# Optimization experiments

Hardware: AMD Instinct MI355X
Metric: run time of the kernel (lower is better)

## Reference

```python
import jax, jax.numpy as jnp
import numpy as np

N_NODES = 100000
D_IN = 64
D_OUT = 64
N_EDGES = 1250000


def setup_inputs() -> dict:
    key = jax.random.key(0)
    k_x, k_e, k_wl, k_bl, k_wr = jax.random.split(key, 5)
    x = jax.random.normal(k_x, (N_NODES, D_IN), dtype=jnp.float32)
    edge_index = jax.random.randint(k_e, (2, N_EDGES), 0, N_NODES, dtype=jnp.int64)
    # SAGEConv params: lin_l (neighbor transform, with bias), lin_r (root transform, no bias)
    s_in = 1.0 / np.sqrt(D_IN)
    W_l = jax.random.uniform(k_wl, (D_IN, D_OUT), dtype=jnp.float32, minval=-s_in, maxval=s_in)
    b_l = jax.random.uniform(k_bl, (D_OUT,), dtype=jnp.float32, minval=-s_in, maxval=s_in)
    W_r = jax.random.uniform(k_wr, (D_IN, D_OUT), dtype=jnp.float32, minval=-s_in, maxval=s_in)
    return {"x": x, "edge_index": edge_index, "W_l": W_l, "b_l": b_l, "W_r": W_r}


def reference(x, edge_index, W_l, b_l, W_r):
    # PyG SAGEConv with aggr='add':
    #   out = lin_l(sum_{j in N(i)} x_j) + lin_r(x_i), then tanh
    src = edge_index[0]  # message sources (x_j)
    dst = edge_index[1]  # message targets (i)
    msg = x[src]                                             # [E, D_IN] gather
    aggr = jax.ops.segment_sum(msg, dst, num_segments=x.shape[0])  # [N, D_IN] scatter-add
    out = aggr @ W_l + b_l + x @ W_r                         # [N, D_OUT]
    return jnp.tanh(out)
```

## Files before the change

kernel.cpp:

```cpp
#include <hip/hip_runtime.h>
#include <hip/hip_bf16.h>
#include <hip/hip_fp16.h>

#define N_NODES 100000
#define D 64
#define N_EDGES 1250000

#define RB 64
#define NB 1563
#define FCAP 1536
#define SORT_CAP 1536

#define CB_SHIFT 11
#define NCB 49
#define CCAP 28672
#define FINE_PER_COARSE 32

#define CPAD 16

#define EPB 8192
#define PARTA_BLOCKS ((N_EDGES + EPB - 1) / EPB)
#define SEGS 16
#define SEG_CAP 1792

#define TNP 256
#define PRE_BLOCKS ((N_NODES + TNP - 1) / TNP)
#define FUSED_BLOCKS (PARTA_BLOCKS + PRE_BLOCKS)

#define NWAVE 16

#define XP 72
#define SMEM_BYTES 55296

#define SG_BPB 2
#define SG_BLOCKS ((NB + SG_BPB - 1) / SG_BPB)

typedef unsigned short ushort_t;
typedef _Float16 half_t;
typedef __attribute__((ext_vector_type(8))) _Float16 half8;
typedef __attribute__((ext_vector_type(4))) float floatx4;

__global__ __launch_bounds__(1024) void pre_part_kernel(
    const float* __restrict__ x, const float* __restrict__ W_l,
    const float* __restrict__ b_l, const float* __restrict__ W_r,
    ushort_t* __restrict__ y, ushort_t* __restrict__ z,
    const int* __restrict__ src, const int* __restrict__ dst,
    int* __restrict__ ccursor, unsigned* __restrict__ coarse,
    int N, int E)
{
    extern __shared__ char smem[];
    int t = threadIdx.x;

    if (blockIdx.x < PARTA_BLOCKS) {
        int* hist16       = (int*)smem;
        int* lbase        = (int*)(smem + 3200);
        int* gbase        = (int*)(smem + 3456);
        int* lwb          = (int*)(smem + 3712);
        unsigned* sortedL = (unsigned*)(smem + 6912);
        const int w = t >> 6;

        if (t < NWAVE * NCB) hist16[t] = 0;
        __syncthreads();

        int base = blockIdx.x * EPB;
        int lim = E - base; if (lim > EPB) lim = EPB;

        for (int i = t; i < lim; i += 1024)
            atomicAdd(&hist16[w * NCB + (dst[base + i] >> CB_SHIFT)], 1);
        __syncthreads();

        if (t < 64) {
            int cw[NWAVE]; int tot = 0;
            if (t < NCB) {
#pragma unroll
                for (int k = 0; k < NWAVE; k++) { cw[k] = hist16[k * NCB + t]; tot += cw[k]; }
            }
            int inc = tot;
#pragma unroll
            for (int off = 1; off < 64; off <<= 1) {
                int n = __shfl_up(inc, off, 64);
                if (t >= off) inc += n;
            }
            int ex = inc - tot;
            if (t < NCB) {
                lbase[t] = ex;
                gbase[t] = tot ? atomicAdd(&ccursor[t * CPAD], tot) : 0;
                int run = ex;
#pragma unroll
                for (int k = 0; k < NWAVE; k++) { lwb[k * NCB + t] = run; run += cw[k]; }
            } else {
                lbase[t] = lim;
            }
        }
        __syncthreads();

        for (int i = t; i < lim; i += 1024) {
            int d = dst[base + i];
            int s = src[base + i];
            int b = d >> CB_SHIFT;
            int pos = atomicSub(&hist16[w * NCB + b], 1) - 1;
            sortedL[lwb[w * NCB + b] + pos] =
                (unsigned)s | ((unsigned)(d & ((1 << CB_SHIFT) - 1)) << 17);
        }
        __syncthreads();

        for (int i = t; i < lim; i += 1024) {
            int lo = 0;
#pragma unroll
            for (int s2 = 32; s2; s2 >>= 1) {
                int c = lo + s2;
                if (c < 64 && lbase[c] <= i) lo = c;
            }
            coarse[(size_t)lo * CCAP + gbase[lo] + (i - lbase[lo])] = sortedL[i];
        }
        return;
    }

    half_t* sWt = (half_t*)smem;
    half_t* sXh = (half_t*)(smem + 18432);

    for (int i = t; i < 64 * 64; i += 1024) {
        int k = i >> 6, c = i & 63;
        sWt[c * XP + k]        = (half_t)W_l[i];
        sWt[(64 + c) * XP + k] = (half_t)W_r[i];
    }

    long base = (long)(blockIdx.x - PARTA_BLOCKS) * TNP;
    for (int i = t; i < TNP * 16; i += 1024) {
        int n = i >> 4, q = i & 15;
        long node = base + n;
        float4 v = make_float4(0.f, 0.f, 0.f, 0.f);
        if (node < N) v = ((const float4*)(x + node * D))[q];
        half_t* p = &sXh[n * XP + q * 4];
        p[0] = (half_t)v.x; p[1] = (half_t)v.y;
        p[2] = (half_t)v.z; p[3] = (half_t)v.w;
    }
    __syncthreads();

    const int lane  = t & 63;
    const int w     = t >> 6;
    const int col16 = lane & 15;
    const int quad  = lane >> 4;

    const int nrow = w * 16 + col16;
    half8 xb0 = *(half8*)&sXh[nrow * XP + quad * 8];
    half8 xb1 = *(half8*)&sXh[nrow * XP + 32 + quad * 8];

    float4 bq[4];
#pragma unroll
    for (int j = 0; j < 4; j++) bq[j] = *(const float4*)(b_l + j * 16 + quad * 4);

#pragma unroll
    for (int ct = 0; ct < 4; ct++) {
        int c = ct * 16 + col16;
        half8 wa0 = *(half8*)&sWt[c * XP + quad * 8];
        half8 wa1 = *(half8*)&sWt[c * XP + 32 + quad * 8];
        floatx4 acc = {0.f, 0.f, 0.f, 0.f};
        acc = __builtin_amdgcn_mfma_f32_16x16x32_f16(wa0, xb0, acc, 0, 0, 0);
        acc = __builtin_amdgcn_mfma_f32_16x16x32_f16(wa1, xb1, acc, 0, 0, 0);
        union { half_t h[4]; uint2 u; } pk;
        pk.h[0] = (half_t)acc[0]; pk.h[1] = (half_t)acc[1];
        pk.h[2] = (half_t)acc[2]; pk.h[3] = (half_t)acc[3];
        *(uint2*)&sXh[nrow * XP + ct * 16 + quad * 4] = pk.u;
    }
    __syncthreads();

    for (int c2 = t; c2 < TNP * 8; c2 += 1024) {
        int row = c2 >> 3, f = c2 & 7;
        if (base + row < N)
            *(uint4*)(y + (base + row) * D + f * 8) = *(uint4*)&sXh[row * XP + f * 8];
    }
    __syncthreads();

#pragma unroll
    for (int ct = 4; ct < 8; ct++) {
        int c = ct * 16 + col16;
        half8 wa0 = *(half8*)&sWt[c * XP + quad * 8];
        half8 wa1 = *(half8*)&sWt[c * XP + 32 + quad * 8];
        floatx4 acc = {0.f, 0.f, 0.f, 0.f};
        acc = __builtin_amdgcn_mfma_f32_16x16x32_f16(wa0, xb0, acc, 0, 0, 0);
        acc = __builtin_amdgcn_mfma_f32_16x16x32_f16(wa1, xb1, acc, 0, 0, 0);
        float4 bv = bq[ct - 4];
        union { half_t h[4]; uint2 u; } pk;
        pk.h[0] = (half_t)(acc[0] + bv.x); pk.h[1] = (half_t)(acc[1] + bv.y);
        pk.h[2] = (half_t)(acc[2] + bv.z); pk.h[3] = (half_t)(acc[3] + bv.w);
        *(uint2*)&sXh[nrow * XP + (ct - 4) * 16 + quad * 4] = pk.u;
    }
    __syncthreads();

    for (int c2 = t; c2 < TNP * 8; c2 += 1024) {
        int row = c2 >> 3, f = c2 & 7;
        if (base + row < N)
            *(uint4*)(z + (base + row) * D + f * 8) = *(uint4*)&sXh[row * XP + f * 8];
    }
}

__global__ __launch_bounds__(256) void partB_kernel(
    const unsigned* __restrict__ coarse, const int* __restrict__ ccursor,
    int* __restrict__ fcursor, unsigned* __restrict__ fine)
{
    __shared__ int hist4[4 * FINE_PER_COARSE];
    __shared__ int lbase2[FINE_PER_COARSE];
    __shared__ int gbase2[FINE_PER_COARSE];
    __shared__ int lwb2[4 * FINE_PER_COARSE];
    __shared__ unsigned sortedL[SEG_CAP];

    int cb = blockIdx.x >> 4;
    int seg = blockIdx.x & 15;
    int t = threadIdx.x;
    const int w = t >> 6;

    int cnt = ccursor[cb * CPAD];
    int segLen = (cnt + SEGS - 1) / SEGS;
    int beg = seg * segLen;
    int end = beg + segLen; if (end > cnt) end = cnt;
    int lim = end - beg; if (lim < 0) lim = 0;

    if (t < 4 * FINE_PER_COARSE) hist4[t] = 0;
    __syncthreads();

    const unsigned* __restrict__ slab = coarse + (size_t)cb * CCAP + beg;

    for (int i = t; i < lim; i += 256)
        atomicAdd(&hist4[w * FINE_PER_COARSE + ((slab[i] >> 17) >> 6)], 1);
    __syncthreads();

    if (t < 64) {
        int c0 = 0, c1 = 0, c2 = 0, c3 = 0, tot = 0;
        if (t < FINE_PER_COARSE) {
            c0 = hist4[t]; c1 = hist4[FINE_PER_COARSE + t];
            c2 = hist4[2 * FINE_PER_COARSE + t]; c3 = hist4[3 * FINE_PER_COARSE + t];
            tot = c0 + c1 + c2 + c3;
        }
        int inc = tot;
#pragma unroll
        for (int off = 1; off < 32; off <<= 1) {
            int n = __shfl_up(inc, off, 64);
            if (t >= off) inc += n;
        }
        int ex = inc - tot;
        if (t < FINE_PER_COARSE) {
            lbase2[t] = ex;
            int fb = cb * FINE_PER_COARSE + t;
            gbase2[t] = tot ? atomicAdd(&fcursor[fb * CPAD], tot) : 0;
            lwb2[t]                       = ex;
            lwb2[FINE_PER_COARSE + t]     = ex + c0;
            lwb2[2 * FINE_PER_COARSE + t] = ex + c0 + c1;
            lwb2[3 * FINE_PER_COARSE + t] = ex + c0 + c1 + c2;
        }
    }
    __syncthreads();

    for (int i = t; i < lim; i += 256) {
        unsigned e = slab[i];
        unsigned cl = e >> 17;
        int loc = cl >> 6;
        int pos = atomicSub(&hist4[w * FINE_PER_COARSE + loc], 1) - 1;
        sortedL[lwb2[w * FINE_PER_COARSE + loc] + pos] =
            (e & 0x1FFFFu) | ((cl & 63u) << 17);
    }
    __syncthreads();

    for (int i = t; i < lim; i += 256) {
        int lo = 0;
#pragma unroll
        for (int s2 = 16; s2; s2 >>= 1) {
            int c = lo + s2;
            if (c < FINE_PER_COARSE && lbase2[c] <= i) lo = c;
        }
        fine[((size_t)cb * FINE_PER_COARSE + lo) * FCAP + gbase2[lo] + (i - lbase2[lo])]
            = sortedL[i];
    }
}

__global__ __launch_bounds__(512) void sortgather_kernel(
    const ushort_t* __restrict__ y, const ushort_t* __restrict__ z,
    const unsigned* __restrict__ part, const int* __restrict__ cursor,
    float* __restrict__ out, int N)
{
    __shared__ int sorted[SORT_CAP];
    __shared__ int hist[RB];
    __shared__ int cur[RB];
    __shared__ int begL[RB];

    int t = threadIdx.x;

    for (int sub = 0; sub < SG_BPB; sub++) {
        int b = blockIdx.x * SG_BPB + sub;
        if (b >= NB) break;
        __syncthreads();

        int cnt = cursor[b * CPAD];
        if (cnt > SORT_CAP) cnt = SORT_CAP;
        const unsigned* __restrict__ slab = part + (size_t)b * FCAP;

        unsigned e0 = 0, e1 = 0, e2 = 0;
        int i0 = t, i1 = t + 512, i2 = t + 1024;
        if (i0 < cnt) e0 = slab[i0];
        if (i1 < cnt) e1 = slab[i1];
        if (i2 < cnt) e2 = slab[i2];

        if (t < RB) hist[t] = 0;
        __syncthreads();

        if (i0 < cnt) atomicAdd(&hist[e0 >> 17], 1);
        if (i1 < cnt) atomicAdd(&hist[e1 >> 17], 1);
        if (i2 < cnt) atomicAdd(&hist[e2 >> 17], 1);
        __syncthreads();

        if (t < RB) {
            int v = hist[t];
            int inc = v;
#pragma unroll
            for (int off = 1; off < RB; off <<= 1) {
                int n = __shfl_up(inc, off, RB);
                if (t >= off) inc += n;
            }
            int ex = inc - v;
            cur[t] = ex;
            begL[t] = ex;
        }
        __syncthreads();

        if (i0 < cnt) { int p = atomicAdd(&cur[e0 >> 17], 1); sorted[p] = (int)(e0 & 0x1FFFF); }
        if (i1 < cnt) { int p = atomicAdd(&cur[e1 >> 17], 1); sorted[p] = (int)(e1 & 0x1FFFF); }
        if (i2 < cnt) { int p = atomicAdd(&cur[e2 >> 17], 1); sorted[p] = (int)(e2 & 0x1FFFF); }
        __syncthreads();

        const int g = t >> 3;
        const int f = t & 7;
        int myBeg = begL[g];
        int myDeg = hist[g];

        float2 acc0 = make_float2(0.f, 0.f), acc1 = acc0, acc2 = acc0, acc3 = acc0;

#define ACC(r) { \
        float2 c0 = __half22float2(*(const __half2*)&(r).x); \
        float2 c1 = __half22float2(*(const __half2*)&(r).y); \
        float2 c2 = __half22float2(*(const __half2*)&(r).z); \
        float2 c3 = __half22float2(*(const __half2*)&(r).w); \
        acc0.x += c0.x; acc0.y += c0.y; acc1.x += c1.x; acc1.y += c1.y; \
        acc2.x += c2.x; acc2.y += c2.y; acc3.x += c3.x; acc3.y += c3.y; }

        int i = 0;
        for (; i + 8 <= myDeg; i += 8) {
            int s0 = sorted[myBeg + i];
            int s1 = sorted[myBeg + i + 1];
            int s2 = sorted[myBeg + i + 2];
            int s3 = sorted[myBeg + i + 3];
            int s4 = sorted[myBeg + i + 4];
            int s5 = sorted[myBeg + i + 5];
            int s6 = sorted[myBeg + i + 6];
            int s7 = sorted[myBeg + i + 7];
            uint4 r0 = ((const uint4*)(y + (size_t)s0 * D))[f];
            uint4 r1 = ((const uint4*)(y + (size_t)s1 * D))[f];
            uint4 r2 = ((const uint4*)(y + (size_t)s2 * D))[f];
            uint4 r3 = ((const uint4*)(y + (size_t)s3 * D))[f];
            uint4 r4 = ((const uint4*)(y + (size_t)s4 * D))[f];
            uint4 r5 = ((const uint4*)(y + (size_t)s5 * D))[f];
            uint4 r6 = ((const uint4*)(y + (size_t)s6 * D))[f];
            uint4 r7 = ((const uint4*)(y + (size_t)s7 * D))[f];
            ACC(r0) ACC(r1) ACC(r2) ACC(r3) ACC(r4) ACC(r5) ACC(r6) ACC(r7)
        }
        for (; i + 4 <= myDeg; i += 4) {
            int s0 = sorted[myBeg + i];
            int s1 = sorted[myBeg + i + 1];
            int s2 = sorted[myBeg + i + 2];
            int s3 = sorted[myBeg + i + 3];
            uint4 r0 = ((const uint4*)(y + (size_t)s0 * D))[f];
            uint4 r1 = ((const uint4*)(y + (size_t)s1 * D))[f];
            uint4 r2 = ((const uint4*)(y + (size_t)s2 * D))[f];
            uint4 r3 = ((const uint4*)(y + (size_t)s3 * D))[f];
            ACC(r0) ACC(r1) ACC(r2) ACC(r3)
        }
        for (; i < myDeg; i++) {
            int s = sorted[myBeg + i];
            uint4 r = ((const uint4*)(y + (size_t)s * D))[f];
            ACC(r)
        }
#undef ACC

        long gn = (long)b * RB + g;
        if (gn < N) {
            uint4 zr = ((const uint4*)(z + (size_t)gn * D))[f];
            float2 z0 = __half22float2(*(const __half2*)&zr.x);
            float2 z1 = __half22float2(*(const __half2*)&zr.y);
            float2 z2 = __half22float2(*(const __half2*)&zr.z);
            float2 z3 = __half22float2(*(const __half2*)&zr.w);
            float4 o0, o1;
            o0.x = tanhf(acc0.x + z0.x); o0.y = tanhf(acc0.y + z0.y);
            o0.z = tanhf(acc1.x + z1.x); o0.w = tanhf(acc1.y + z1.y);
            o1.x = tanhf(acc2.x + z2.x); o1.y = tanhf(acc2.y + z2.y);
            o1.z = tanhf(acc3.x + z3.x); o1.w = tanhf(acc3.y + z3.y);
            float4* op = (float4*)(out + gn * D);
            op[2 * f] = o0;
            op[2 * f + 1] = o1;
        }
    }
}

extern "C" void kernel_launch(void* const* d_in, const int* in_sizes, int n_in,
                              void* d_out, int out_size, void* d_ws, size_t ws_size,
                              hipStream_t stream) {
    const float* x   = (const float*)d_in[0];
    const int* ei    = (const int*)d_in[1];
    const float* W_l = (const float*)d_in[2];
    const float* b_l = (const float*)d_in[3];
    const float* W_r = (const float*)d_in[4];
    float* out = (float*)d_out;

    const int N = N_NODES;
    const int E = N_EDGES;
    const int* src = ei;
    const int* dst = ei + E;

    char* ws = (char*)d_ws;
    ushort_t* y      = (ushort_t*)(ws);
    ushort_t* z      = (ushort_t*)(ws + 12800000);
    unsigned* coarse = (unsigned*)(ws + 25600000);
    unsigned* fine   = (unsigned*)(ws + 31219712);
    int* ccursor     = (int*)(ws + 40822784);
    int* fcursor     = (int*)(ws + 40825920);

    hipMemsetAsync(ccursor, 0, 103168, stream);

    pre_part_kernel<<<FUSED_BLOCKS, 1024, SMEM_BYTES, stream>>>(
        x, W_l, b_l, W_r, y, z, src, dst, ccursor, coarse, N, E);
    partB_kernel<<<NCB * SEGS, 256, 0, stream>>>(coarse, ccursor, fcursor, fine);
    sortgather_kernel<<<SG_BLOCKS, 512, 0, stream>>>(y, z, fine, fcursor, out, N);
}
```

Before: 138.7 us.

## Scatter coarse partition directly to global and make pre-GEMM wave-local

```diff
diff --git a/kernel.cpp b/kernel.cpp
--- a/kernel.cpp
+++ b/kernel.cpp
@@ -26,7 +26,6 @@
 #define TNP 256
 #define PRE_BLOCKS ((N_NODES + TNP - 1) / TNP)
 #define FUSED_BLOCKS (PARTA_BLOCKS + PRE_BLOCKS)
-
 #define NWAVE 16
 
 #define XP 72
@@ -52,11 +51,8 @@
     int t = threadIdx.x;
 
     if (blockIdx.x < PARTA_BLOCKS) {
-        int* hist16       = (int*)smem;
-        int* lbase        = (int*)(smem + 3200);
-        int* gbase        = (int*)(smem + 3456);
-        int* lwb          = (int*)(smem + 3712);
-        unsigned* sortedL = (unsigned*)(smem + 6912);
+        int* hist16 = (int*)smem;
+        int* lwb16  = (int*)(smem + 3200);
         const int w = t >> 6;
 
         if (t < NWAVE * NCB) hist16[t] = 0;
@@ -69,28 +65,13 @@
             atomicAdd(&hist16[w * NCB + (dst[base + i] >> CB_SHIFT)], 1);
         __syncthreads();
 
-        if (t < 64) {
+        if (t < NCB) {
             int cw[NWAVE]; int tot = 0;
-            if (t < NCB) {
-#pragma unroll
-                for (int k = 0; k < NWAVE; k++) { cw[k] = hist16[k * NCB + t]; tot += cw[k]; }
-            }
-            int inc = tot;
-#pragma unroll
-            for (int off = 1; off < 64; off <<= 1) {
-                int n = __shfl_up(inc, off, 64);
-                if (t >= off) inc += n;
-            }
-            int ex = inc - tot;
-            if (t < NCB) {
-                lbase[t] = ex;
-                gbase[t] = tot ? atomicAdd(&ccursor[t * CPAD], tot) : 0;
-                int run = ex;
-#pragma unroll
-                for (int k = 0; k < NWAVE; k++) { lwb[k * NCB + t] = run; run += cw[k]; }
-            } else {
-                lbase[t] = lim;
-            }
+#pragma unroll
+            for (int k = 0; k < NWAVE; k++) { cw[k] = hist16[k * NCB + t]; tot += cw[k]; }
+            int g = tot ? atomicAdd(&ccursor[t * CPAD], tot) : 0;
+#pragma unroll
+            for (int k = 0; k < NWAVE; k++) { lwb16[k * NCB + t] = g; g += cw[k]; }
         }
         __syncthreads();
 
@@ -99,19 +80,8 @@
             int s = src[base + i];
             int b = d >> CB_SHIFT;
             int pos = atomicSub(&hist16[w * NCB + b], 1) - 1;
-            sortedL[lwb[w * NCB + b] + pos] =
+            coarse[(size_t)b * CCAP + lwb16[w * NCB + b] + pos] =
                 (unsigned)s | ((unsigned)(d & ((1 << CB_SHIFT) - 1)) << 17);
-        }
-        __syncthreads();
-
-        for (int i = t; i < lim; i += 1024) {
-            int lo = 0;
-#pragma unroll
-            for (int s2 = 32; s2; s2 >>= 1) {
-                int c = lo + s2;
-                if (c < 64 && lbase[c] <= i) lo = c;
-            }
-            coarse[(size_t)lo * CCAP + gbase[lo] + (i - lbase[lo])] = sortedL[i];
         }
         return;
     }
@@ -125,30 +95,38 @@
         sWt[(64 + c) * XP + k] = (half_t)W_r[i];
     }
 
-    long base = (long)(blockIdx.x - PARTA_BLOCKS) * TNP;
-    for (int i = t; i < TNP * 16; i += 1024) {
-        int n = i >> 4, q = i & 15;
-        long node = base + n;
-        float4 v = make_float4(0.f, 0.f, 0.f, 0.f);
-        if (node < N) v = ((const float4*)(x + node * D))[q];
-        half_t* p = &sXh[n * XP + q * 4];
-        p[0] = (half_t)v.x; p[1] = (half_t)v.y;
-        p[2] = (half_t)v.z; p[3] = (half_t)v.w;
-    }
-    __syncthreads();
-
     const int lane  = t & 63;
     const int w     = t >> 6;
     const int col16 = lane & 15;
     const int quad  = lane >> 4;
 
+    float4 bq[4];
+#pragma unroll
+    for (int j = 0; j < 4; j++) bq[j] = *(const float4*)(b_l + j * 16 + quad * 4);
+
+    __syncthreads();
+
+    long base = (long)(blockIdx.x - PARTA_BLOCKS) * TNP;
+
+    {
+        int rl = w * 16 + (lane >> 2);
+        long node = base + rl;
+        bool ok = node < N;
+        int qb = lane & 3;
+#pragma unroll
+        for (int k = 0; k < 4; k++) {
+            int q = qb + k * 4;
+            float4 v = make_float4(0.f, 0.f, 0.f, 0.f);
+            if (ok) v = ((const float4*)(x + node * D))[q];
+            half_t* p = &sXh[rl * XP + q * 4];
+            p[0] = (half_t)v.x; p[1] = (half_t)v.y;
+            p[2] = (half_t)v.z; p[3] = (half_t)v.w;
+        }
+    }
+
     const int nrow = w * 16 + col16;
     half8 xb0 = *(half8*)&sXh[nrow * XP + quad * 8];
     half8 xb1 = *(half8*)&sXh[nrow * XP + 32 + quad * 8];
-
-    float4 bq[4];
-#pragma unroll
-    for (int j = 0; j < 4; j++) bq[j] = *(const float4*)(b_l + j * 16 + quad * 4);
 
 #pragma unroll
     for (int ct = 0; ct < 4; ct++) {
@@ -163,14 +141,17 @@
         pk.h[2] = (half_t)acc[2]; pk.h[3] = (half_t)acc[3];
         *(uint2*)&sXh[nrow * XP + ct * 16 + quad * 4] = pk.u;
     }
-    __syncthreads();
-
-    for (int c2 = t; c2 < TNP * 8; c2 += 1024) {
-        int row = c2 >> 3, f = c2 & 7;
-        if (base + row < N)
-            *(uint4*)(y + (base + row) * D + f * 8) = *(uint4*)&sXh[row * XP + f * 8];
-    }
-    __syncthreads();
+
+    {
+        int rl = w * 16 + (lane >> 3);
+        int f = lane & 7;
+#pragma unroll
+        for (int it = 0; it < 2; it++) {
+            int row = rl + it * 8;
+            if (base + row < N)
+                *(uint4*)(y + (base + row) * D + f * 8) = *(uint4*)&sXh[row * XP + f * 8];
+        }
+    }
 
 #pragma unroll
     for (int ct = 4; ct < 8; ct++) {
@@ -186,12 +167,16 @@
         pk.h[2] = (half_t)(acc[2] + bv.z); pk.h[3] = (half_t)(acc[3] + bv.w);
         *(uint2*)&sXh[nrow * XP + (ct - 4) * 16 + quad * 4] = pk.u;
     }
-    __syncthreads();
-
-    for (int c2 = t; c2 < TNP * 8; c2 += 1024) {
-        int row = c2 >> 3, f = c2 & 7;
-        if (base + row < N)
-            *(uint4*)(z + (base + row) * D + f * 8) = *(uint4*)&sXh[row * XP + f * 8];
+
+    {
+        int rl = w * 16 + (lane >> 3);
+        int f = lane & 7;
+#pragma unroll
+        for (int it = 0; it < 2; it++) {
+            int row = rl + it * 8;
+            if (base + row < N)
+                *(uint4*)(z + (base + row) * D + f * 8) = *(uint4*)&sXh[row * XP + f * 8];
+        }
     }
 }
 
@@ -331,6 +316,10 @@
         const int f = t & 7;
         int myBeg = begL[g];
         int myDeg = hist[g];
+
+        long gn = (long)b * RB + g;
+        uint4 zr = make_uint4(0u, 0u, 0u, 0u);
+        if (gn < N) zr = ((const uint4*)(z + (size_t)gn * D))[f];
 
         float2 acc0 = make_float2(0.f, 0.f), acc1 = acc0, acc2 = acc0, acc3 = acc0;
 
@@ -380,9 +369,7 @@
         }
 #undef ACC
 
-        long gn = (long)b * RB + g;
         if (gn < N) {
-            uint4 zr = ((const uint4*)(z + (size_t)gn * D))[f];
             float2 z0 = __half22float2(*(const __half2*)&zr.x);
             float2 z1 = __half22float2(*(const __half2*)&zr.y);
             float2 z2 = __half22float2(*(const __half2*)&zr.z);
```

Measured after the change: 143.4 us. 1.03x slower.
